# Kernel tuning notes

Hardware: AMD Instinct MI355X
Metric: run time of the kernel (lower is better)

Reference implementation:

```python
import jax, jax.numpy as jnp
import numpy as np

NUM_HEADS = 8

def setup_inputs() -> dict:
    key = jax.random.key(0)
    k1, k2, k3, k4, k5 = jax.random.split(key, 5)
    B, N, C = 4, 2048, 512
    x = jax.random.normal(k1, (B, N, C), dtype=jnp.float32)
    s = 1.0 / np.sqrt(C)
    qkv_w = jax.random.uniform(k2, (3 * C, C), dtype=jnp.float32, minval=-s, maxval=s)
    qkv_b = jax.random.uniform(k3, (3 * C,), dtype=jnp.float32, minval=-s, maxval=s)
    proj_w = jax.random.uniform(k4, (C, C), dtype=jnp.float32, minval=-s, maxval=s)
    proj_b = jax.random.uniform(k5, (C,), dtype=jnp.float32, minval=-s, maxval=s)
    return {"x": x, "qkv_w": qkv_w, "qkv_b": qkv_b, "proj_w": proj_w, "proj_b": proj_b}

def reference(x, qkv_w, qkv_b, proj_w, proj_b):
    B, N, C = x.shape
    H = NUM_HEADS
    D = C // H
    scale = D ** -0.5
    # qkv: [B,N,3C] -> [3,B,H,N,D]
    qkv = (jnp.einsum('bnc,oc->bno', x, qkv_w) + qkv_b)
    qkv = qkv.reshape(B, N, 3, H, D).transpose(2, 0, 3, 1, 4)
    q, k, v = qkv[0], qkv[1], qkv[2]
    attn = jnp.einsum('bhnd,bhmd->bhnm', q, k) * scale  # [B,H,N,N]
    attn = jax.nn.softmax(attn, axis=-1)
    out = jnp.einsum('bhnm,bhmd->bhnd', attn, v)  # [B,H,N,D]
    out = out.transpose(0, 2, 1, 3).reshape(B, N, C)
    return jnp.einsum('bnc,oc->bno', out, proj_w) + proj_b
```

## Files before the change

kernel.cpp:

```cpp
#include <hip/hip_runtime.h>
#include <stdint.h>


typedef short bf16x8 __attribute__((ext_vector_type(8)));
typedef float f32x2  __attribute__((ext_vector_type(2)));
typedef float f32x4  __attribute__((ext_vector_type(4)));
typedef float f32x16 __attribute__((ext_vector_type(16)));
typedef unsigned int u32x4 __attribute__((ext_vector_type(4)));

__device__ __forceinline__ unsigned short f2bf(float f) {
    unsigned int u = __builtin_bit_cast(unsigned int, f);
    u += 0x7fffu + ((u >> 16) & 1u);
    return (unsigned short)(u >> 16);
}
__device__ __forceinline__ unsigned int pk2(float a, float b) {
    return (unsigned int)f2bf(a) | ((unsigned int)f2bf(b) << 16);
}
__device__ __forceinline__ float fexp2(float x) {
    return __builtin_amdgcn_exp2f(x);
}
__device__ __forceinline__ bf16x8 ld8_f32(const float* __restrict__ p) {
    float4 f0 = *(const float4*)p;
    float4 f1 = *(const float4*)(p + 4);
    u32x4 u = {pk2(f0.x, f0.y), pk2(f0.z, f0.w), pk2(f1.x, f1.y), pk2(f1.z, f1.w)};
    return __builtin_bit_cast(bf16x8, u);
}
__device__ __forceinline__ void async16(const void* g, void* l) {
    __builtin_amdgcn_global_load_lds(
        (const __attribute__((address_space(1))) unsigned int*)g,
        (__attribute__((address_space(3))) unsigned int*)l,
        16, 0, 0);
}

#define MFMA16(a, b, c) __builtin_amdgcn_mfma_f32_16x16x32_bf16((a), (b), (c), 0, 0, 0)
#define MFMA32(a, b, c) __builtin_amdgcn_mfma_f32_32x32x16_bf16((a), (b), (c), 0, 0, 0)

__global__ void cvt_bf16(const float* __restrict__ x,
                         const float* __restrict__ w,
                         const float* __restrict__ w2,
                         unsigned short* __restrict__ xb,
                         unsigned short* __restrict__ wb,
                         unsigned short* __restrict__ wb2)
{
    const int G = 524288 + 98304 + 32768;
    for (int idx = blockIdx.x * 256 + threadIdx.x; idx < G; idx += gridDim.x * 256) {
        if (idx < 524288)
            *(bf16x8*)(xb + (size_t)idx * 8) = ld8_f32(x + (size_t)idx * 8);
        else if (idx < 524288 + 98304) {
            int j = idx - 524288;
            *(bf16x8*)(wb + (size_t)j * 8) = ld8_f32(w + (size_t)j * 8);
        } else {
            int j = idx - 524288 - 98304;
            *(bf16x8*)(wb2 + (size_t)j * 8) = ld8_f32(w2 + (size_t)j * 8);
        }
    }
}

__global__ __launch_bounds__(256, 4)
void gemm_qkv(const unsigned short* __restrict__ A,
              const unsigned short* __restrict__ B,
              const float* __restrict__ bias,
              unsigned short* __restrict__ out0,
              unsigned short* __restrict__ out1,
              unsigned short* __restrict__ out2,
              int K)
{
    __shared__ unsigned short sA[128 * 32];
    __shared__ unsigned short sB[128 * 32];

    const int tid  = threadIdx.x;
    const int wave = tid >> 6, lane = tid & 63;
    const int l = lane & 15, q16 = lane >> 4;
    const int wm = wave >> 1, wn = wave & 1;
    const int bid = blockIdx.x;
    const int slot = bid >> 3;
    const int m0 = ((bid & 7) * 8 + slot / 12) * 128;
    const int n0 = (slot % 12) * 128;

    f32x4 acc[4][4];
#pragma unroll
    for (int i = 0; i < 4; ++i)
#pragma unroll
        for (int j = 0; j < 4; ++j)
            acc[i][j] = (f32x4){0.f, 0.f, 0.f, 0.f};

    for (int k0 = 0; k0 < K; k0 += 32) {
#pragma unroll
        for (int call = 0; call < 2; ++call) {
            int L = call * 256 + tid;
            int r = L >> 2, c = L & 3;
            async16(A + (size_t)(m0 + r) * K + k0 + c * 8, sA + L * 8);
            async16(B + (size_t)(n0 + r) * K + k0 + c * 8, sB + L * 8);
        }
        __syncthreads();

        bf16x8 af[4], bfr[4];
#pragma unroll
        for (int i = 0; i < 4; ++i)
            af[i] = *(const bf16x8*)(sA + ((wm * 64 + i * 16 + l) * 4 + q16) * 8);
#pragma unroll
        for (int j = 0; j < 4; ++j)
            bfr[j] = *(const bf16x8*)(sB + ((wn * 64 + j * 16 + l) * 4 + q16) * 8);
#pragma unroll
        for (int i = 0; i < 4; ++i)
#pragma unroll
            for (int j = 0; j < 4; ++j)
                acc[i][j] = MFMA16(af[i], bfr[j], acc[i][j]);
        __syncthreads();
    }

    const float lscale = 0.18033688f;
#pragma unroll
    for (int i = 0; i < 4; ++i) {
#pragma unroll
        for (int j = 0; j < 4; ++j) {
            int col = n0 + wn * 64 + j * 16 + l;
            float bv = bias[col];
#pragma unroll
            for (int r = 0; r < 4; ++r) {
                int row = m0 + wm * 64 + i * 16 + q16 * 4 + r;
                float val = acc[i][j][r] + bv;
                int which = col >> 9;
                int h = (col >> 6) & 7, d = col & 63;
                int b = row >> 11, n = row & 2047;
                if (which == 0)
                    out0[(size_t)(((b * 8 + h) * 2048) + n) * 64 + d] = f2bf(val * lscale);
                else if (which == 1)
                    out1[(size_t)(((b * 8 + h) * 2048) + n) * 64 + d] = f2bf(val);
                else {
                    int np = (n & ~12) | ((n & 8) >> 1) | ((n & 4) << 1);
                    out2[(size_t)(((b * 8 + h) * 64) + d) * 2048 + np] = f2bf(val);
                }
            }
        }
    }
}

__global__ __launch_bounds__(256, 4)
void gemm_out(const unsigned short* __restrict__ A,
              const unsigned short* __restrict__ B,
              const float* __restrict__ bias,
              float* __restrict__ outf,
              int K, int N)
{
    __shared__ unsigned short sA[64 * 32];
    __shared__ unsigned short sB[128 * 32];

    const int tid  = threadIdx.x;
    const int wave = tid >> 6, lane = tid & 63;
    const int l = lane & 15, q16 = lane >> 4;
    const int wm = wave >> 1, wn = wave & 1;
    const int bid = blockIdx.x;
    const int slot = bid >> 3;
    const int m0 = ((bid & 7) * 16 + (slot >> 2)) * 64;
    const int n0 = (slot & 3) * 128;

    f32x4 acc[2][4];
#pragma unroll
    for (int i = 0; i < 2; ++i)
#pragma unroll
        for (int j = 0; j < 4; ++j)
            acc[i][j] = (f32x4){0.f, 0.f, 0.f, 0.f};

    for (int k0 = 0; k0 < K; k0 += 32) {
        {
            int r = tid >> 2, c = tid & 3;
            async16(A + (size_t)(m0 + r) * K + k0 + c * 8, sA + tid * 8);
        }
#pragma unroll
        for (int call = 0; call < 2; ++call) {
            int L = call * 256 + tid;
            int r = L >> 2, c = L & 3;
            async16(B + (size_t)(n0 + r) * K + k0 + c * 8, sB + L * 8);
        }
        __syncthreads();

        bf16x8 af[2], bfr[4];
#pragma unroll
        for (int i = 0; i < 2; ++i)
            af[i] = *(const bf16x8*)(sA + ((wm * 32 + i * 16 + l) * 4 + q16) * 8);
#pragma unroll
        for (int j = 0; j < 4; ++j)
            bfr[j] = *(const bf16x8*)(sB + ((wn * 64 + j * 16 + l) * 4 + q16) * 8);
#pragma unroll
        for (int i = 0; i < 2; ++i)
#pragma unroll
            for (int j = 0; j < 4; ++j)
                acc[i][j] = MFMA16(af[i], bfr[j], acc[i][j]);
        __syncthreads();
    }

#pragma unroll
    for (int i = 0; i < 2; ++i) {
#pragma unroll
        for (int j = 0; j < 4; ++j) {
            int col = n0 + wn * 64 + j * 16 + l;
            float bv = bias[col];
#pragma unroll
            for (int r = 0; r < 4; ++r) {
                int row = m0 + wm * 32 + i * 16 + q16 * 4 + r;
                outf[(size_t)row * N + col] = acc[i][j][r] + bv;
            }
        }
    }
}

__global__ __launch_bounds__(128, 1)
void attn_fused(const unsigned short* __restrict__ Q,
                const unsigned short* __restrict__ Km,
                const unsigned short* __restrict__ Vt,
                unsigned short* __restrict__ O)
{
    __shared__ unsigned short sK[2][128 * 64];
    __shared__ unsigned short sVt[2][64 * 128];

    const int tid  = threadIdx.x;
    const int wave = tid >> 6, lane = tid & 63;
    const int l31 = lane & 31, h = lane >> 5;
    const int swz = l31 & 7;
    const int bid = blockIdx.x;
    const int slot = bid >> 3;
    const int bh = (bid & 7) * 4 + (slot >> 4);
    const int n0 = (slot & 15) * 128;
    const int q0 = n0 + wave * 64;

    const unsigned short* Kp = Km + (size_t)bh * 2048 * 64;
    const unsigned short* Vp = Vt + (size_t)bh * 64 * 2048;
    const unsigned short* sKf = &sK[0][0];
    const unsigned short* sVf = &sVt[0][0];

    int ka[4], va[2][2];
#pragma unroll
    for (int ks = 0; ks < 4; ++ks)
        ka[ks] = l31 * 64 + ((ks * 2 + h) ^ swz) * 8;
#pragma unroll
    for (int m1 = 0; m1 < 2; ++m1)
#pragma unroll
        for (int ks2 = 0; ks2 < 2; ++ks2)
            va[m1][ks2] = l31 * 128 + ((m1 * 4 + ks2 * 2 + h) ^ swz) * 8;

    int ksrc[8], vsrc[8], dst[8];
#pragma unroll
    for (int c = 0; c < 8; ++c) {
        int s = c * 128 + tid;
        int rk = s >> 3;
        ksrc[c] = rk * 64 + ((s & 7) ^ (rk & 7)) * 8;
        int rv = s >> 4;
        vsrc[c] = rv * 2048 + ((s & 15) ^ (rv & 7)) * 8;
        dst[c] = s * 8;
    }

    bf16x8 qf[2][4];
#pragma unroll
    for (int qt = 0; qt < 2; ++qt)
#pragma unroll
        for (int ks = 0; ks < 4; ++ks)
            qf[qt][ks] = *(const bf16x8*)(Q + (size_t)(bh * 2048 + q0 + qt * 32 + l31) * 64
                                          + ks * 16 + h * 8);

    f32x16 oacc[2][2];
#pragma unroll
    for (int qt = 0; qt < 2; ++qt)
#pragma unroll
        for (int dt = 0; dt < 2; ++dt)
#pragma unroll
            for (int e = 0; e < 16; ++e) oacc[qt][dt][e] = 0.f;
    f32x16 Zv;
#pragma unroll
    for (int e = 0; e < 16; ++e) Zv[e] = 0.f;
    f32x2 l2[2];
    l2[0] = (f32x2){0.f, 0.f};
    l2[1] = (f32x2){0.f, 0.f};

#pragma unroll
    for (int c = 0; c < 8; ++c) {
        async16(Kp + ksrc[c], (void*)(sKf + dst[c]));
        async16(Vp + vsrc[c], (void*)(sVf + dst[c]));
    }
    __syncthreads();

    for (int it = 0; it < 16; ++it) {
        const int nb = ((it + 1) & 1) * 8192;
        if (it < 15) {
            int kv = (it + 1) * 128;
#pragma unroll
            for (int c = 0; c < 8; ++c)
                async16(Kp + (size_t)kv * 64 + ksrc[c], (void*)(sKf + nb + dst[c]));
        }

        f32x16 sacc[2][4];
#pragma unroll
        for (int mt = 0; mt < 4; ++mt) {
            bf16x8 kf0 = *(const bf16x8*)(sKf + ka[0] + mt * 2048);
            sacc[0][mt] = MFMA32(kf0, qf[0][0], Zv);
            sacc[1][mt] = MFMA32(kf0, qf[1][0], Zv);
#pragma unroll
            for (int ks = 1; ks < 4; ++ks) {
                bf16x8 kf = *(const bf16x8*)(sKf + ka[ks] + mt * 2048);
                sacc[0][mt] = MFMA32(kf, qf[0][ks], sacc[0][mt]);
                sacc[1][mt] = MFMA32(kf, qf[1][ks], sacc[1][mt]);
            }
        }

        if (it < 15) {
            int kv = (it + 1) * 128;
#pragma unroll
            for (int c = 0; c < 8; ++c)
                async16(Vp + (size_t)kv + vsrc[c], (void*)(sVf + nb + dst[c]));
        }

#pragma unroll
        for (int mt = 0; mt < 4; ++mt) {
            unsigned int pk[2][4][2];
#pragma unroll
            for (int qt = 0; qt < 2; ++qt) {
#pragma unroll
                for (int g = 0; g < 4; ++g) {
                    float p0 = fexp2(sacc[qt][mt][4 * g + 0]);
                    float p1 = fexp2(sacc[qt][mt][4 * g + 1]);
                    float p2 = fexp2(sacc[qt][mt][4 * g + 2]);
                    float p3 = fexp2(sacc[qt][mt][4 * g + 3]);
                    l2[qt] += (f32x2){p0, p1};
                    l2[qt] += (f32x2){p2, p3};
                    pk[qt][g][0] = __builtin_amdgcn_perm(
                        __builtin_bit_cast(unsigned int, p1),
                        __builtin_bit_cast(unsigned int, p0), 0x07060302u);
                    pk[qt][g][1] = __builtin_amdgcn_perm(
                        __builtin_bit_cast(unsigned int, p3),
                        __builtin_bit_cast(unsigned int, p2), 0x07060302u);
                }
            }
#pragma unroll
            for (int ks2 = 0; ks2 < 2; ++ks2) {
                u32x4 bu0, bu1;
                bu0[0] = pk[0][2 * ks2][0];
                bu0[1] = pk[0][2 * ks2][1];
                bu0[2] = pk[0][2 * ks2 + 1][0];
                bu0[3] = pk[0][2 * ks2 + 1][1];
                bu1[0] = pk[1][2 * ks2][0];
                bu1[1] = pk[1][2 * ks2][1];
                bu1[2] = pk[1][2 * ks2 + 1][0];
                bu1[3] = pk[1][2 * ks2 + 1][1];
                bf16x8 bf0 = __builtin_bit_cast(bf16x8, bu0);
                bf16x8 bf1 = __builtin_bit_cast(bf16x8, bu1);
#pragma unroll
                for (int dt = 0; dt < 2; ++dt) {
                    bf16x8 vf = *(const bf16x8*)(sVf + va[mt & 1][ks2]
                                                 + (mt >> 1) * 64 + dt * 4096);
                    oacc[0][dt] = MFMA32(vf, bf0, oacc[0][dt]);
                    oacc[1][dt] = MFMA32(vf, bf1, oacc[1][dt]);
                }
            }
        }

#pragma unroll
        for (int ks = 0; ks < 4; ++ks) ka[ks] ^= 8192;
        va[0][0] ^= 8192; va[0][1] ^= 8192; va[1][0] ^= 8192; va[1][1] ^= 8192;
        __syncthreads();
    }

    const int b = bh >> 3, hh = bh & 7;
#pragma unroll
    for (int qt = 0; qt < 2; ++qt) {
        float l_run = l2[qt][0] + l2[qt][1];
        l_run += __shfl_xor(l_run, 32);
        float inv = 1.f / fmaxf(l_run, 1e-20f);
        unsigned short* obase = O + ((size_t)(b * 2048 + q0 + qt * 32 + l31)) * 512 + hh * 64;
#pragma unroll
        for (int dt = 0; dt < 2; ++dt)
#pragma unroll
            for (int g = 0; g < 4; ++g) {
                int d = dt * 32 + 8 * g + 4 * h;
                unsigned int w0 = pk2(oacc[qt][dt][4 * g + 0] * inv,
                                      oacc[qt][dt][4 * g + 1] * inv);
                unsigned int w1 = pk2(oacc[qt][dt][4 * g + 2] * inv,
                                      oacc[qt][dt][4 * g + 3] * inv);
                uint2 w = {w0, w1};
                *(uint2*)(obase + d) = w;
            }
    }
}

extern "C" void kernel_launch(void* const* d_in, const int* in_sizes, int n_in,
                              void* d_out, int out_size, void* d_ws, size_t ws_size,
                              hipStream_t stream)
{
    const float* x      = (const float*)d_in[0];
    const float* qkv_w  = (const float*)d_in[1];
    const float* qkv_b  = (const float*)d_in[2];
    const float* proj_w = (const float*)d_in[3];
    const float* proj_b = (const float*)d_in[4];

    const size_t PER = 4u * 8u * 2048u * 64u;
    unsigned short* q_ws  = (unsigned short*)d_ws;
    unsigned short* k_ws  = q_ws  + PER;
    unsigned short* vt_ws = k_ws  + PER;
    unsigned short* ao_ws = vt_ws + PER;
    unsigned short* wb2   = ao_ws + PER;

    unsigned short* xb = (unsigned short*)d_out;
    unsigned short* wb = xb + PER;

    cvt_bf16<<<dim3(640), 256, 0, stream>>>(x, qkv_w, proj_w, xb, wb, wb2);
    gemm_qkv<<<dim3(768), 256, 0, stream>>>(xb, wb, qkv_b, q_ws, k_ws, vt_ws, 512);
    attn_fused<<<dim3(512), 128, 0, stream>>>(q_ws, k_ws, vt_ws, ao_ws);
    gemm_out<<<dim3(512), 256, 0, stream>>>(ao_ws, wb2, proj_b, (float*)d_out, 512, 512);
}
```

Before: 169.9 us.

## Split attention KV tiles across two wave pairs and reduce partials in LDS

```diff
diff --git a/kernel.cpp b/kernel.cpp
--- a/kernel.cpp
+++ b/kernel.cpp
@@ -205,7 +205,7 @@
     }
 }
 
-__global__ __launch_bounds__(128, 1)
+__global__ __launch_bounds__(256, 2)
 void attn_fused(const unsigned short* __restrict__ Q,
                 const unsigned short* __restrict__ Km,
                 const unsigned short* __restrict__ Vt,
@@ -218,11 +218,12 @@
     const int wave = tid >> 6, lane = tid & 63;
     const int l31 = lane & 31, h = lane >> 5;
     const int swz = l31 & 7;
+    const int qh = wave & 1, kh = wave >> 1;
     const int bid = blockIdx.x;
     const int slot = bid >> 3;
     const int bh = (bid & 7) * 4 + (slot >> 4);
     const int n0 = (slot & 15) * 128;
-    const int q0 = n0 + wave * 64;
+    const int q0 = n0 + qh * 64;
 
     const unsigned short* Kp = Km + (size_t)bh * 2048 * 64;
     const unsigned short* Vp = Vt + (size_t)bh * 64 * 2048;
@@ -232,17 +233,17 @@
     int ka[4], va[2][2];
 #pragma unroll
     for (int ks = 0; ks < 4; ++ks)
-        ka[ks] = l31 * 64 + ((ks * 2 + h) ^ swz) * 8;
+        ka[ks] = (kh * 64 + l31) * 64 + ((ks * 2 + h) ^ swz) * 8;
 #pragma unroll
     for (int m1 = 0; m1 < 2; ++m1)
 #pragma unroll
         for (int ks2 = 0; ks2 < 2; ++ks2)
-            va[m1][ks2] = l31 * 128 + ((m1 * 4 + ks2 * 2 + h) ^ swz) * 8;
-
-    int ksrc[8], vsrc[8], dst[8];
-#pragma unroll
-    for (int c = 0; c < 8; ++c) {
-        int s = c * 128 + tid;
+            va[m1][ks2] = l31 * 128 + ((m1 * 4 + ks2 * 2 + h) ^ swz) * 8 + kh * 64;
+
+    int ksrc[4], vsrc[4], dst[4];
+#pragma unroll
+    for (int c = 0; c < 4; ++c) {
+        int s = wave * 256 + c * 64 + lane;
         int rk = s >> 3;
         ksrc[c] = rk * 64 + ((s & 7) ^ (rk & 7)) * 8;
         int rv = s >> 4;
@@ -273,7 +274,7 @@
     l2[1] = (f32x2){0.f, 0.f};
 
 #pragma unroll
-    for (int c = 0; c < 8; ++c) {
+    for (int c = 0; c < 4; ++c) {
         async16(Kp + ksrc[c], (void*)(sKf + dst[c]));
         async16(Vp + vsrc[c], (void*)(sVf + dst[c]));
     }
@@ -284,13 +285,13 @@
         if (it < 15) {
             int kv = (it + 1) * 128;
 #pragma unroll
-            for (int c = 0; c < 8; ++c)
+            for (int c = 0; c < 4; ++c)
                 async16(Kp + (size_t)kv * 64 + ksrc[c], (void*)(sKf + nb + dst[c]));
         }
 
-        f32x16 sacc[2][4];
-#pragma unroll
-        for (int mt = 0; mt < 4; ++mt) {
+        f32x16 sacc[2][2];
+#pragma unroll
+        for (int mt = 0; mt < 2; ++mt) {
             bf16x8 kf0 = *(const bf16x8*)(sKf + ka[0] + mt * 2048);
             sacc[0][mt] = MFMA32(kf0, qf[0][0], Zv);
             sacc[1][mt] = MFMA32(kf0, qf[1][0], Zv);
@@ -305,12 +306,12 @@
         if (it < 15) {
             int kv = (it + 1) * 128;
 #pragma unroll
-            for (int c = 0; c < 8; ++c)
+            for (int c = 0; c < 4; ++c)
                 async16(Vp + (size_t)kv + vsrc[c], (void*)(sVf + nb + dst[c]));
         }
 
 #pragma unroll
-        for (int mt = 0; mt < 4; ++mt) {
+        for (int mt = 0; mt < 2; ++mt) {
             unsigned int pk[2][4][2];
 #pragma unroll
             for (int qt = 0; qt < 2; ++qt) {
@@ -345,8 +346,7 @@
                 bf16x8 bf1 = __builtin_bit_cast(bf16x8, bu1);
 #pragma unroll
                 for (int dt = 0; dt < 2; ++dt) {
-                    bf16x8 vf = *(const bf16x8*)(sVf + va[mt & 1][ks2]
-                                                 + (mt >> 1) * 64 + dt * 4096);
+                    bf16x8 vf = *(const bf16x8*)(sVf + va[mt][ks2] + dt * 4096);
                     oacc[0][dt] = MFMA32(vf, bf0, oacc[0][dt]);
                     oacc[1][dt] = MFMA32(vf, bf1, oacc[1][dt]);
                 }
@@ -359,25 +359,55 @@
         __syncthreads();
     }
 
-    const int b = bh >> 3, hh = bh & 7;
-#pragma unroll
-    for (int qt = 0; qt < 2; ++qt) {
-        float l_run = l2[qt][0] + l2[qt][1];
-        l_run += __shfl_xor(l_run, 32);
-        float inv = 1.f / fmaxf(l_run, 1e-20f);
-        unsigned short* obase = O + ((size_t)(b * 2048 + q0 + qt * 32 + l31)) * 512 + hh * 64;
-#pragma unroll
-        for (int dt = 0; dt < 2; ++dt)
-#pragma unroll
-            for (int g = 0; g < 4; ++g) {
-                int d = dt * 32 + 8 * g + 4 * h;
-                unsigned int w0 = pk2(oacc[qt][dt][4 * g + 0] * inv,
-                                      oacc[qt][dt][4 * g + 1] * inv);
-                unsigned int w1 = pk2(oacc[qt][dt][4 * g + 2] * inv,
-                                      oacc[qt][dt][4 * g + 3] * inv);
-                uint2 w = {w0, w1};
-                *(uint2*)(obase + d) = w;
-            }
+    float* sf = (float*)&sK[0][0];
+    float* sl = (float*)&sVt[0][0];
+    if (kh == 1) {
+        const int base = (qh * 64 + lane) * 64;
+#pragma unroll
+        for (int qt = 0; qt < 2; ++qt)
+#pragma unroll
+            for (int dt = 0; dt < 2; ++dt) {
+                int chunk = (qt * 2 + dt) ^ (lane & 3);
+                *(f32x16*)(sf + base + chunk * 16) = oacc[qt][dt];
+            }
+        *(f32x2*)(sl + (qh * 64 + lane) * 4 + 0) = l2[0];
+        *(f32x2*)(sl + (qh * 64 + lane) * 4 + 2) = l2[1];
+    }
+    __syncthreads();
+    if (kh == 0) {
+        const int base = (qh * 64 + lane) * 64;
+#pragma unroll
+        for (int qt = 0; qt < 2; ++qt)
+#pragma unroll
+            for (int dt = 0; dt < 2; ++dt) {
+                int chunk = (qt * 2 + dt) ^ (lane & 3);
+                f32x16 part = *(const f32x16*)(sf + base + chunk * 16);
+#pragma unroll
+                for (int e = 0; e < 16; ++e) oacc[qt][dt][e] += part[e];
+            }
+        l2[0] += *(const f32x2*)(sl + (qh * 64 + lane) * 4 + 0);
+        l2[1] += *(const f32x2*)(sl + (qh * 64 + lane) * 4 + 2);
+
+        const int b = bh >> 3, hh = bh & 7;
+#pragma unroll
+        for (int qt = 0; qt < 2; ++qt) {
+            float l_run = l2[qt][0] + l2[qt][1];
+            l_run += __shfl_xor(l_run, 32);
+            float inv = 1.f / fmaxf(l_run, 1e-20f);
+            unsigned short* obase = O + ((size_t)(b * 2048 + q0 + qt * 32 + l31)) * 512 + hh * 64;
+#pragma unroll
+            for (int dt = 0; dt < 2; ++dt)
+#pragma unroll
+                for (int g = 0; g < 4; ++g) {
+                    int d = dt * 32 + 8 * g + 4 * h;
+                    unsigned int w0 = pk2(oacc[qt][dt][4 * g + 0] * inv,
+                                          oacc[qt][dt][4 * g + 1] * inv);
+                    unsigned int w1 = pk2(oacc[qt][dt][4 * g + 2] * inv,
+                                          oacc[qt][dt][4 * g + 3] * inv);
+                    uint2 w = {w0, w1};
+                    *(uint2*)(obase + d) = w;
+                }
+        }
     }
 }
 
@@ -403,6 +433,6 @@
 
     cvt_bf16<<<dim3(640), 256, 0, stream>>>(x, qkv_w, proj_w, xb, wb, wb2);
     gemm_qkv<<<dim3(768), 256, 0, stream>>>(xb, wb, qkv_b, q_ws, k_ws, vt_ws, 512);
-    attn_fused<<<dim3(512), 128, 0, stream>>>(q_ws, k_ws, vt_ws, ao_ws);
+    attn_fused<<<dim3(512), 256, 0, stream>>>(q_ws, k_ws, vt_ws, ao_ws);
     gemm_out<<<dim3(512), 256, 0, stream>>>(ao_ws, wb2, proj_b, (float*)d_out, 512, 512);
 }
```

Result: faster. 156.0 us (-8.2%).
